# Optimization experiments

Hardware: AMD Instinct MI355X
Metric: run time of the kernel (lower is better)

The kernel has to match this reference:

```python
import jax, jax.numpy as jnp
import numpy as np

N_EXPERTS = 8
TOP_K = 2
D_MODEL = 1024
D_FF = 4 * D_MODEL

def setup_inputs() -> dict:
    key = jax.random.key(0)
    ks = jax.random.split(key, 5)
    s_in = 1.0 / np.sqrt(D_MODEL)
    s_ff = 1.0 / np.sqrt(D_FF)
    return {
        "x": jax.random.normal(ks[0], (2, 2048, D_MODEL), dtype=jnp.float32),
        "Wr": jax.random.normal(ks[1], (N_EXPERTS, D_MODEL), dtype=jnp.float32) * s_in,
        "W1": jax.random.normal(ks[2], (N_EXPERTS, D_FF, D_MODEL), dtype=jnp.float32) * s_in,
        "W2": jax.random.normal(ks[3], (N_EXPERTS, D_MODEL, D_FF), dtype=jnp.float32) * s_ff,
        "W3": jax.random.normal(ks[4], (N_EXPERTS, D_FF, D_MODEL), dtype=jnp.float32) * s_in,
    }

def reference(x, Wr, W1, W2, W3):
    B, S, D = x.shape
    T = B * S
    xf = x.reshape(T, D)
    logits = xf @ Wr.T                         # [T, E]
    probs = jax.nn.softmax(logits, axis=-1)
    top_p, top_i = jax.lax.top_k(probs, TOP_K)  # [T, K]
    top_p = top_p / jnp.sum(top_p, axis=-1, keepdims=True)
    # per-token combine weight for each expert: [T, E]
    onehot = jax.nn.one_hot(top_i, N_EXPERTS, dtype=x.dtype)  # [T, K, E]
    cw = jnp.einsum('tke,tk->te', onehot, top_p)
    out = jnp.zeros_like(xf)
    for e in range(N_EXPERTS):  # fixed small structural loop over experts
        h = jax.nn.silu(xf @ W1[e].T) * (xf @ W3[e].T)  # [T, F]
        y = h @ W2[e].T                                 # [T, D]
        out = out + cw[:, e:e+1] * y
    importance = jnp.sum(probs, axis=0)                 # [E]
    load = jnp.sum(jnp.sum(onehot, axis=1), axis=0)     # [E]
    aux_loss = jnp.sum(importance * load) * (N_EXPERTS / (T ** 2 + 1e-06))
    return out.reshape(B, S, D), aux_loss
```

## Files before the change

### kernel.cpp

```cpp
#include <hip/hip_runtime.h>

#define T_TOK 4096
#define DM 1024
#define DF 4096
#define NE 8
#define BM 128
#define BK 64
#define RCAP 9216
#define MAXT 72
#define CHUNK_B 8192
#define ACH_B 16384

typedef _Float16 f16x8 __attribute__((ext_vector_type(8)));
typedef float f32x4 __attribute__((ext_vector_type(4)));

#define MFMA16(a, b, c) __builtin_amdgcn_mfma_f32_16x16x32_f16(a, b, c, 0, 0, 0)

__device__ __forceinline__ ushort f2h_bits(float f) {
    _Float16 h = (_Float16)f;
    return __builtin_bit_cast(unsigned short, h);
}

__device__ __forceinline__ uint4 pack8(float4 a, float4 b) {
    union { ushort u[8]; uint4 v; } r;
    r.u[0] = f2h_bits(a.x); r.u[1] = f2h_bits(a.y);
    r.u[2] = f2h_bits(a.z); r.u[3] = f2h_bits(a.w);
    r.u[4] = f2h_bits(b.x); r.u[5] = f2h_bits(b.y);
    r.u[6] = f2h_bits(b.z); r.u[7] = f2h_bits(b.w);
    return r.v;
}

__device__ __forceinline__ void gll16(const void* g, void* l) {
    __builtin_amdgcn_global_load_lds(
        (const __attribute__((address_space(1))) unsigned int*)g,
        (__attribute__((address_space(3))) unsigned int*)l, 16, 0, 0);
}

__global__ __launch_bounds__(256) void k_init(float* __restrict__ out,
                                              int* __restrict__ misc,
                                              int* __restrict__ row_tok) {
    int i = blockIdx.x * 256 + threadIdx.x;
    if (i < T_TOK * DM + 1) out[i] = 0.f;
    if (i < RCAP) row_tok[i] = -1;
    if (i < 256) misc[i] = 0;
}

__global__ __launch_bounds__(64) void k_router(const float* __restrict__ x,
                                               const float* __restrict__ Wr,
                                               float* __restrict__ probs,
                                               int* __restrict__ topi,
                                               float* __restrict__ topw,
                                               int* __restrict__ cnt) {
    int t = blockIdx.x;
    int lane = threadIdx.x;
    const float* xr = x + (size_t)t * DM;
    float s[NE];
#pragma unroll
    for (int e = 0; e < NE; e++) s[e] = 0.f;
    for (int j = lane; j < DM; j += 64) {
        float xv = xr[j];
#pragma unroll
        for (int e = 0; e < NE; e++) s[e] += xv * Wr[e * DM + j];
    }
#pragma unroll
    for (int off = 32; off > 0; off >>= 1) {
#pragma unroll
        for (int e = 0; e < NE; e++) s[e] += __shfl_xor(s[e], off, 64);
    }
    if (lane == 0) {
        float mx = s[0];
#pragma unroll
        for (int e = 1; e < NE; e++) mx = fmaxf(mx, s[e]);
        float ex[NE], sum = 0.f;
#pragma unroll
        for (int e = 0; e < NE; e++) { ex[e] = expf(s[e] - mx); sum += ex[e]; }
        float inv = 1.f / sum;
        float p[NE];
#pragma unroll
        for (int e = 0; e < NE; e++) { p[e] = ex[e] * inv; probs[t * NE + e] = p[e]; }
        int i0 = 0;
#pragma unroll
        for (int e = 1; e < NE; e++) if (p[e] > p[i0]) i0 = e;
        int i1 = (i0 == 0) ? 1 : 0;
#pragma unroll
        for (int e = 0; e < NE; e++) if (e != i0 && p[e] > p[i1]) i1 = e;
        float w0 = p[i0], w1 = p[i1], winv = 1.f / (w0 + w1);
        topi[2 * t] = i0;     topw[2 * t] = w0 * winv;
        topi[2 * t + 1] = i1; topw[2 * t + 1] = w1 * winv;
        atomicAdd(&cnt[i0], 1);
        atomicAdd(&cnt[i1], 1);
    }
}

__global__ __launch_bounds__(256) void k_scan(const float* __restrict__ probs,
                                              const int* __restrict__ cnt,
                                              int* __restrict__ poff,
                                              int* __restrict__ texp,
                                              float* __restrict__ aux_out) {
    __shared__ float red[256 * NE];
    int tid = threadIdx.x;
    float part[NE];
#pragma unroll
    for (int e = 0; e < NE; e++) part[e] = 0.f;
    for (int t = tid; t < T_TOK; t += 256) {
#pragma unroll
        for (int e = 0; e < NE; e++) part[e] += probs[t * NE + e];
    }
#pragma unroll
    for (int e = 0; e < NE; e++) red[tid * NE + e] = part[e];
    __syncthreads();
    for (int s2 = 128; s2 > 0; s2 >>= 1) {
        if (tid < s2) {
#pragma unroll
            for (int e = 0; e < NE; e++) red[tid * NE + e] += red[(tid + s2) * NE + e];
        }
        __syncthreads();
    }
    if (tid == 0) {
        float al = 0.f;
#pragma unroll
        for (int e = 0; e < NE; e++) al += red[e] * (float)cnt[e];
        *aux_out = al * (8.0f / (16777216.0f + 1e-6f));
        int run = 0, tix = 0;
        for (int e = 0; e < NE; e++) {
            poff[e] = run;
            int nt = (cnt[e] + BM - 1) / BM;
            for (int i = 0; i < nt; i++) texp[tix++] = e;
            run += nt * BM;
        }
    }
}

__global__ __launch_bounds__(256) void k_assign(const int* __restrict__ topi,
                                                const float* __restrict__ topw,
                                                const int* __restrict__ poff,
                                                int* __restrict__ fill,
                                                int* __restrict__ row_tok,
                                                float* __restrict__ row_w) {
    int t = blockIdx.x * 256 + threadIdx.x;
    if (t >= T_TOK) return;
#pragma unroll
    for (int k = 0; k < 2; k++) {
        int e = topi[2 * t + k];
        int pos = atomicAdd(&fill[e], 1);
        int r = poff[e] + pos;
        row_tok[r] = t;
        row_w[r] = topw[2 * t + k];
    }
}

__global__ __launch_bounds__(256) void k_convert(const float* __restrict__ src,
                                                 ushort* __restrict__ dst,
                                                 int row_len) {
    int nk = row_len >> 6;
    int kt = blockIdx.x, rt = blockIdx.y;
    int tid = threadIdx.x;
    int r = tid >> 2, c0 = (tid & 3) * 16;
    const float* s = src + (size_t)(rt * 64 + r) * row_len + kt * 64 + c0;
    float4 v0 = *(const float4*)(s);
    float4 v1 = *(const float4*)(s + 4);
    float4 v2 = *(const float4*)(s + 8);
    float4 v3 = *(const float4*)(s + 12);
    char* chunk = (char*)dst + ((size_t)rt * nk + kt) * CHUNK_B;
    int sw = (r & 7) << 4;
    *(uint4*)(chunk + r * 128 + ((2 * c0) ^ sw)) = pack8(v0, v1);
    *(uint4*)(chunk + r * 128 + ((2 * c0 + 16) ^ sw)) = pack8(v2, v3);
}

__global__ __launch_bounds__(256) void k_gather_t(const float* __restrict__ x,
                                                  const int* __restrict__ row_tok,
                                                  ushort* __restrict__ xg) {
    int kt = blockIdx.x, rt = blockIdx.y;
    int tid = threadIdx.x;
    int r = tid >> 1, c0 = (tid & 1) * 32;
    int tok = row_tok[rt * BM + r];
    char* chunk = (char*)xg + ((size_t)rt * 16 + kt) * ACH_B;
    int sw = (r & 7) << 4;
    if (tok >= 0) {
        const float* s = x + (size_t)tok * DM + kt * 64 + c0;
#pragma unroll
        for (int j = 0; j < 4; j++) {
            float4 va = *(const float4*)(s + j * 8);
            float4 vb = *(const float4*)(s + j * 8 + 4);
            *(uint4*)(chunk + r * 128 + ((2 * (c0 + j * 8)) ^ sw)) = pack8(va, vb);
        }
    } else {
        uint4 z = {0, 0, 0, 0};
#pragma unroll
        for (int j = 0; j < 4; j++)
            *(uint4*)(chunk + r * 128 + ((2 * (c0 + j * 8)) ^ sw)) = z;
    }
}

__global__ __launch_bounds__(256) void k_gemm1_t(const ushort* __restrict__ xg,
                                                 const ushort* __restrict__ W1h,
                                                 const ushort* __restrict__ W3h,
                                                 const int* __restrict__ texp,
                                                 ushort* __restrict__ hbuf) {
    __shared__ __align__(16) char lA[2][16384];
    __shared__ __align__(16) char lB1[2][8192];
    __shared__ __align__(16) char lB3[2][8192];
    int ct = blockIdx.x, rt = blockIdx.y;
    int e = texp[rt];
    const char* Ac  = (const char*)xg + (size_t)rt * 16 * ACH_B;
    const char* B1c = (const char*)W1h + (size_t)((e * 64 + ct) * 16) * CHUNK_B;
    const char* B3c = (const char*)W3h + (size_t)((e * 64 + ct) * 16) * CHUNK_B;
    int tid = threadIdx.x, lane = tid & 63, wv = tid >> 6;
    int wr = wv >> 1, wc = wv & 1;

    const f32x4 fz = {0.f, 0.f, 0.f, 0.f};
    f32x4 acc1[4][2], acc3[4][2];
#pragma unroll
    for (int m = 0; m < 4; m++)
#pragma unroll
        for (int n = 0; n < 2; n++) { acc1[m][n] = fz; acc3[m][n] = fz; }

#define G1_STAGE(kt_, b_)                                                              \
    {                                                                                  \
        const char* As_  = Ac + (kt_) * ACH_B;                                         \
        const char* B1s_ = B1c + (kt_) * CHUNK_B;                                      \
        const char* B3s_ = B3c + (kt_) * CHUNK_B;                                      \
        _Pragma("unroll")                                                              \
        for (int i = 0; i < 4; i++)                                                    \
            gll16(As_ + wv * 4096 + i * 1024 + lane * 16, lA[b_] + wv * 4096 + i * 1024); \
        _Pragma("unroll")                                                              \
        for (int i = 0; i < 2; i++)                                                    \
            gll16(B1s_ + wv * 2048 + i * 1024 + lane * 16, lB1[b_] + wv * 2048 + i * 1024); \
        _Pragma("unroll")                                                              \
        for (int i = 0; i < 2; i++)                                                    \
            gll16(B3s_ + wv * 2048 + i * 1024 + lane * 16, lB3[b_] + wv * 2048 + i * 1024); \
    }

    G1_STAGE(0, 0);
    asm volatile("s_waitcnt vmcnt(0)" ::: "memory");
    __syncthreads();
    int cur = 0;
    for (int kt = 0; kt < 16; kt++) {
        if (kt < 15) G1_STAGE(kt + 1, cur ^ 1);
#pragma unroll
        for (int ks = 0; ks < 2; ks++) {
            int kbyte = (ks * 32 + (lane >> 4) * 8) * 2;
            f16x8 af[4];
#pragma unroll
            for (int m = 0; m < 4; m++) {
                int r = wr * 64 + m * 16 + (lane & 15);
                af[m] = *(const f16x8*)(lA[cur] + r * 128 + (kbyte ^ ((r & 7) << 4)));
            }
#pragma unroll
            for (int n = 0; n < 2; n++) {
                int c = wc * 32 + n * 16 + (lane & 15);
                int off = c * 128 + (kbyte ^ ((c & 7) << 4));
                f16x8 b1 = *(const f16x8*)(lB1[cur] + off);
                f16x8 b3 = *(const f16x8*)(lB3[cur] + off);
#pragma unroll
                for (int m = 0; m < 4; m++) {
                    acc1[m][n] = MFMA16(af[m], b1, acc1[m][n]);
                    acc3[m][n] = MFMA16(af[m], b3, acc3[m][n]);
                }
            }
        }
        asm volatile("s_waitcnt vmcnt(0)" ::: "memory");
        __syncthreads();
        cur ^= 1;
    }
#undef G1_STAGE
    char* hc = (char*)hbuf + (size_t)(rt * 64 + ct) * ACH_B;
#pragma unroll
    for (int m = 0; m < 4; m++) {
#pragma unroll
        for (int i = 0; i < 4; i++) {
            int r = wr * 64 + m * 16 + (lane >> 4) * 4 + i;
            int sw = (r & 7) << 4;
#pragma unroll
            for (int n = 0; n < 2; n++) {
                int f = wc * 32 + n * 16 + (lane & 15);
                float a1 = acc1[m][n][i], a3 = acc3[m][n][i];
                float h = (a1 / (1.f + expf(-a1))) * a3;
                *(ushort*)(hc + r * 128 + ((2 * f) ^ sw)) = f2h_bits(h);
            }
        }
    }
}

__global__ __launch_bounds__(256) void k_gemm2_t(const ushort* __restrict__ hbuf,
                                                 const ushort* __restrict__ W2h,
                                                 const int* __restrict__ texp,
                                                 const int* __restrict__ row_tok,
                                                 const float* __restrict__ row_w,
                                                 float* __restrict__ out) {
    __shared__ __align__(16) char lA[2][16384];
    __shared__ __align__(16) char lB[2][8192];
    int ct = blockIdx.x, rt = blockIdx.y;
    int e = texp[rt];
    const char* Ac = (const char*)hbuf + (size_t)rt * 64 * ACH_B;
    const char* Bc = (const char*)W2h + (size_t)((e * 16 + ct) * 64) * CHUNK_B;
    int tid = threadIdx.x, lane = tid & 63, wv = tid >> 6;
    int wr = wv >> 1, wc = wv & 1;

    const f32x4 fz = {0.f, 0.f, 0.f, 0.f};
    f32x4 acc[4][2];
#pragma unroll
    for (int m = 0; m < 4; m++)
#pragma unroll
        for (int n = 0; n < 2; n++) acc[m][n] = fz;

#define G2_STAGE(kt_, b_)                                                              \
    {                                                                                  \
        const char* As_ = Ac + (kt_) * ACH_B;                                          \
        const char* Bs_ = Bc + (kt_) * CHUNK_B;                                        \
        _Pragma("unroll")                                                              \
        for (int i = 0; i < 4; i++)                                                    \
            gll16(As_ + wv * 4096 + i * 1024 + lane * 16, lA[b_] + wv * 4096 + i * 1024); \
        _Pragma("unroll")                                                              \
        for (int i = 0; i < 2; i++)                                                    \
            gll16(Bs_ + wv * 2048 + i * 1024 + lane * 16, lB[b_] + wv * 2048 + i * 1024); \
    }

    G2_STAGE(0, 0);
    asm volatile("s_waitcnt vmcnt(0)" ::: "memory");
    __syncthreads();
    int cur = 0;
    for (int kt = 0; kt < 64; kt++) {
        if (kt < 63) G2_STAGE(kt + 1, cur ^ 1);
#pragma unroll
        for (int ks = 0; ks < 2; ks++) {
            int kbyte = (ks * 32 + (lane >> 4) * 8) * 2;
            f16x8 af[4];
#pragma unroll
            for (int m = 0; m < 4; m++) {
                int r = wr * 64 + m * 16 + (lane & 15);
                af[m] = *(const f16x8*)(lA[cur] + r * 128 + (kbyte ^ ((r & 7) << 4)));
            }
#pragma unroll
            for (int n = 0; n < 2; n++) {
                int c = wc * 32 + n * 16 + (lane & 15);
                f16x8 b = *(const f16x8*)(lB[cur] + c * 128 + (kbyte ^ ((c & 7) << 4)));
#pragma unroll
                for (int m = 0; m < 4; m++) acc[m][n] = MFMA16(af[m], b, acc[m][n]);
            }
        }
        asm volatile("s_waitcnt vmcnt(0)" ::: "memory");
        __syncthreads();
        cur ^= 1;
    }
#undef G2_STAGE
    int cbase = ct * 64 + wc * 32;
#pragma unroll
    for (int m = 0; m < 4; m++) {
#pragma unroll
        for (int i = 0; i < 4; i++) {
            int rr = rt * BM + wr * 64 + m * 16 + (lane >> 4) * 4 + i;
            int tok = row_tok[rr];
            if (tok >= 0) {
                float w = row_w[rr];
                float* orow = out + (size_t)tok * DM + cbase + (lane & 15);
#pragma unroll
                for (int n = 0; n < 2; n++) atomicAdd(&orow[n * 16], w * acc[m][n][i]);
            }
        }
    }
}

extern "C" void kernel_launch(void* const* d_in, const int* in_sizes, int n_in,
                              void* d_out, int out_size, void* d_ws, size_t ws_size,
                              hipStream_t stream) {
    (void)in_sizes; (void)n_in; (void)out_size; (void)ws_size;
    const float* x  = (const float*)d_in[0];
    const float* Wr = (const float*)d_in[1];
    const float* W1 = (const float*)d_in[2];
    const float* W2 = (const float*)d_in[3];
    const float* W3 = (const float*)d_in[4];
    float* out = (float*)d_out;
    char* ws = (char*)d_ws;

    int* misc = (int*)ws;
    int* cnt  = misc;
    int* fill = misc + 8;
    int* poff = misc + 16;
    int* texp = misc + 24;
    int*    topi    = (int*)(ws + 1024);
    float*  topw    = (float*)(ws + 33792);
    float*  probs   = (float*)(ws + 66560);
    int*    row_tok = (int*)(ws + 197632);
    float*  row_w   = (float*)(ws + 234496);
    ushort* xg      = (ushort*)(ws + 271360);
    ushort* hbuf    = (ushort*)(ws + 19145728);
    ushort* W1h     = (ushort*)(ws + 94643200);
    ushort* W3h     = (ushort*)(ws + 161752064);
    ushort* W2h     = (ushort*)(ws + 228860928);

    k_init<<<(T_TOK * DM + 1 + 255) / 256, 256, 0, stream>>>(out, misc, row_tok);
    k_router<<<T_TOK, 64, 0, stream>>>(x, Wr, probs, topi, topw, cnt);
    k_scan<<<1, 256, 0, stream>>>(probs, cnt, poff, texp, out + (size_t)T_TOK * DM);
    k_assign<<<(T_TOK + 255) / 256, 256, 0, stream>>>(topi, topw, poff, fill, row_tok, row_w);

    k_convert<<<dim3(16, 512), 256, 0, stream>>>(W1, W1h, DM);
    k_convert<<<dim3(16, 512), 256, 0, stream>>>(W3, W3h, DM);
    k_convert<<<dim3(64, 128), 256, 0, stream>>>(W2, W2h, DF);
    k_gather_t<<<dim3(16, MAXT), 256, 0, stream>>>(x, row_tok, xg);
    k_gemm1_t<<<dim3(64, MAXT), 256, 0, stream>>>(xg, W1h, W3h, texp, hbuf);
    k_gemm2_t<<<dim3(16, MAXT), 256, 0, stream>>>(hbuf, W2h, texp, row_tok, row_w, out);
}
```

Before: 746.5 us.

## Widen expert GEMM N-tiles, relax waitcnt pipelining, and raise MFMA priority

GEMM1 moves to 512-thread blocks that each cover 128 FF columns, so every loaded activation tile feeds twice as many columns. GEMM2 doubles the per-wave output width to 64 columns, with a 128-column block tile. Both kernels now wait on only the older load batch (partial vmcnt) before the barrier, so the next stage's prefetch overlaps compute. They also raise wave priority around the MFMA section. The cost is more LDS per block and more accumulator registers in GEMM2, which can reduce occupancy, and the grids shrink to half as many blocks.

```diff
diff --git a/kernel.cpp b/kernel.cpp
--- a/kernel.cpp
+++ b/kernel.cpp
@@ -5,7 +5,6 @@
 #define DF 4096
 #define NE 8
 #define BM 128
-#define BK 64
 #define RCAP 9216
 #define MAXT 72
 #define CHUNK_B 8192
@@ -192,21 +191,23 @@
     }
 }
 
-__global__ __launch_bounds__(256) void k_gemm1_t(const ushort* __restrict__ xg,
-                                                 const ushort* __restrict__ W1h,
-                                                 const ushort* __restrict__ W3h,
-                                                 const int* __restrict__ texp,
-                                                 ushort* __restrict__ hbuf) {
+__global__ __launch_bounds__(512, 2) void k_gemm1_t(const ushort* __restrict__ xg,
+                                                    const ushort* __restrict__ W1h,
+                                                    const ushort* __restrict__ W3h,
+                                                    const int* __restrict__ texp,
+                                                    ushort* __restrict__ hbuf) {
     __shared__ __align__(16) char lA[2][16384];
-    __shared__ __align__(16) char lB1[2][8192];
-    __shared__ __align__(16) char lB3[2][8192];
+    __shared__ __align__(16) char lB1[2][16384];
+    __shared__ __align__(16) char lB3[2][16384];
     int ct = blockIdx.x, rt = blockIdx.y;
     int e = texp[rt];
     const char* Ac  = (const char*)xg + (size_t)rt * 16 * ACH_B;
-    const char* B1c = (const char*)W1h + (size_t)((e * 64 + ct) * 16) * CHUNK_B;
-    const char* B3c = (const char*)W3h + (size_t)((e * 64 + ct) * 16) * CHUNK_B;
+    const char* B1c = (const char*)W1h + (size_t)((e * 64 + ct * 2) * 16) * CHUNK_B;
+    const char* B3c = (const char*)W3h + (size_t)((e * 64 + ct * 2) * 16) * CHUNK_B;
     int tid = threadIdx.x, lane = tid & 63, wv = tid >> 6;
-    int wr = wv >> 1, wc = wv & 1;
+    int wr = wv >> 2, wc = wv & 3;
+    int bch = wv >> 2;
+    int bin = (wv & 3) * 2048;
 
     const f32x4 fz = {0.f, 0.f, 0.f, 0.f};
     f32x4 acc1[4][2], acc3[4][2];
@@ -217,26 +218,31 @@
 
 #define G1_STAGE(kt_, b_)                                                              \
     {                                                                                  \
-        const char* As_  = Ac + (kt_) * ACH_B;                                         \
-        const char* B1s_ = B1c + (kt_) * CHUNK_B;                                      \
-        const char* B3s_ = B3c + (kt_) * CHUNK_B;                                      \
-        _Pragma("unroll")                                                              \
-        for (int i = 0; i < 4; i++)                                                    \
-            gll16(As_ + wv * 4096 + i * 1024 + lane * 16, lA[b_] + wv * 4096 + i * 1024); \
+        const char* As_ = Ac + (kt_) * ACH_B;                                          \
         _Pragma("unroll")                                                              \
         for (int i = 0; i < 2; i++)                                                    \
-            gll16(B1s_ + wv * 2048 + i * 1024 + lane * 16, lB1[b_] + wv * 2048 + i * 1024); \
+            gll16(As_ + wv * 2048 + i * 1024 + lane * 16, lA[b_] + wv * 2048 + i * 1024); \
+        const char* B1s_ = B1c + (size_t)(bch * 16 + (kt_)) * CHUNK_B + bin;           \
         _Pragma("unroll")                                                              \
         for (int i = 0; i < 2; i++)                                                    \
-            gll16(B3s_ + wv * 2048 + i * 1024 + lane * 16, lB3[b_] + wv * 2048 + i * 1024); \
+            gll16(B1s_ + i * 1024 + lane * 16, lB1[b_] + wv * 2048 + i * 1024);        \
+        const char* B3s_ = B3c + (size_t)(bch * 16 + (kt_)) * CHUNK_B + bin;           \
+        _Pragma("unroll")                                                              \
+        for (int i = 0; i < 2; i++)                                                    \
+            gll16(B3s_ + i * 1024 + lane * 16, lB3[b_] + wv * 2048 + i * 1024);        \
     }
 
     G1_STAGE(0, 0);
-    asm volatile("s_waitcnt vmcnt(0)" ::: "memory");
-    __syncthreads();
     int cur = 0;
     for (int kt = 0; kt < 16; kt++) {
-        if (kt < 15) G1_STAGE(kt + 1, cur ^ 1);
+        if (kt < 15) {
+            G1_STAGE(kt + 1, cur ^ 1);
+            asm volatile("s_waitcnt vmcnt(6)" ::: "memory");
+        } else {
+            asm volatile("s_waitcnt vmcnt(0)" ::: "memory");
+        }
+        __syncthreads();
+        __builtin_amdgcn_s_setprio(1);
 #pragma unroll
         for (int ks = 0; ks < 2; ks++) {
             int kbyte = (ks * 32 + (lane >> 4) * 8) * 2;
@@ -259,24 +265,24 @@
                 }
             }
         }
-        asm volatile("s_waitcnt vmcnt(0)" ::: "memory");
+        __builtin_amdgcn_s_setprio(0);
         __syncthreads();
         cur ^= 1;
     }
 #undef G1_STAGE
-    char* hc = (char*)hbuf + (size_t)(rt * 64 + ct) * ACH_B;
 #pragma unroll
     for (int m = 0; m < 4; m++) {
 #pragma unroll
         for (int i = 0; i < 4; i++) {
-            int r = wr * 64 + m * 16 + (lane >> 4) * 4 + i;
-            int sw = (r & 7) << 4;
+            int rl = wr * 64 + m * 16 + (lane >> 4) * 4 + i;
+            int sw = (rl & 7) << 4;
 #pragma unroll
             for (int n = 0; n < 2; n++) {
-                int f = wc * 32 + n * 16 + (lane & 15);
+                int fl = wc * 32 + n * 16 + (lane & 15);
                 float a1 = acc1[m][n][i], a3 = acc3[m][n][i];
                 float h = (a1 / (1.f + expf(-a1))) * a3;
-                *(ushort*)(hc + r * 128 + ((2 * f) ^ sw)) = f2h_bits(h);
+                char* hc = (char*)hbuf + ((size_t)rt * 64 + ct * 2 + (fl >> 6)) * ACH_B;
+                *(ushort*)(hc + rl * 128 + ((2 * (fl & 63)) ^ sw)) = f2h_bits(h);
             }
         }
     }
@@ -289,39 +295,46 @@
                                                  const float* __restrict__ row_w,
                                                  float* __restrict__ out) {
     __shared__ __align__(16) char lA[2][16384];
-    __shared__ __align__(16) char lB[2][8192];
+    __shared__ __align__(16) char lB[2][16384];
     int ct = blockIdx.x, rt = blockIdx.y;
     int e = texp[rt];
     const char* Ac = (const char*)hbuf + (size_t)rt * 64 * ACH_B;
-    const char* Bc = (const char*)W2h + (size_t)((e * 16 + ct) * 64) * CHUNK_B;
+    const char* Bc = (const char*)W2h + (size_t)((e * 16 + ct * 2) * 64) * CHUNK_B;
     int tid = threadIdx.x, lane = tid & 63, wv = tid >> 6;
     int wr = wv >> 1, wc = wv & 1;
+    int bch = wv >> 1;
+    int bin = (wv & 1) * 4096;
 
     const f32x4 fz = {0.f, 0.f, 0.f, 0.f};
-    f32x4 acc[4][2];
+    f32x4 acc[4][4];
 #pragma unroll
     for (int m = 0; m < 4; m++)
 #pragma unroll
-        for (int n = 0; n < 2; n++) acc[m][n] = fz;
+        for (int n = 0; n < 4; n++) acc[m][n] = fz;
 
 #define G2_STAGE(kt_, b_)                                                              \
     {                                                                                  \
         const char* As_ = Ac + (kt_) * ACH_B;                                          \
-        const char* Bs_ = Bc + (kt_) * CHUNK_B;                                        \
         _Pragma("unroll")                                                              \
         for (int i = 0; i < 4; i++)                                                    \
             gll16(As_ + wv * 4096 + i * 1024 + lane * 16, lA[b_] + wv * 4096 + i * 1024); \
+        const char* Bs_ = Bc + (size_t)(bch * 64 + (kt_)) * CHUNK_B + bin;             \
         _Pragma("unroll")                                                              \
-        for (int i = 0; i < 2; i++)                                                    \
-            gll16(Bs_ + wv * 2048 + i * 1024 + lane * 16, lB[b_] + wv * 2048 + i * 1024); \
+        for (int i = 0; i < 4; i++)                                                    \
+            gll16(Bs_ + i * 1024 + lane * 16, lB[b_] + wv * 4096 + i * 1024);          \
     }
 
     G2_STAGE(0, 0);
-    asm volatile("s_waitcnt vmcnt(0)" ::: "memory");
-    __syncthreads();
     int cur = 0;
     for (int kt = 0; kt < 64; kt++) {
-        if (kt < 63) G2_STAGE(kt + 1, cur ^ 1);
+        if (kt < 63) {
+            G2_STAGE(kt + 1, cur ^ 1);
+            asm volatile("s_waitcnt vmcnt(8)" ::: "memory");
+        } else {
+            asm volatile("s_waitcnt vmcnt(0)" ::: "memory");
+        }
+        __syncthreads();
+        __builtin_amdgcn_s_setprio(1);
 #pragma unroll
         for (int ks = 0; ks < 2; ks++) {
             int kbyte = (ks * 32 + (lane >> 4) * 8) * 2;
@@ -332,19 +345,19 @@
                 af[m] = *(const f16x8*)(lA[cur] + r * 128 + (kbyte ^ ((r & 7) << 4)));
             }
 #pragma unroll
-            for (int n = 0; n < 2; n++) {
-                int c = wc * 32 + n * 16 + (lane & 15);
+            for (int n = 0; n < 4; n++) {
+                int c = wc * 64 + n * 16 + (lane & 15);
                 f16x8 b = *(const f16x8*)(lB[cur] + c * 128 + (kbyte ^ ((c & 7) << 4)));
 #pragma unroll
                 for (int m = 0; m < 4; m++) acc[m][n] = MFMA16(af[m], b, acc[m][n]);
             }
         }
-        asm volatile("s_waitcnt vmcnt(0)" ::: "memory");
+        __builtin_amdgcn_s_setprio(0);
         __syncthreads();
         cur ^= 1;
     }
 #undef G2_STAGE
-    int cbase = ct * 64 + wc * 32;
+    int cbase = ct * 128 + wc * 64;
 #pragma unroll
     for (int m = 0; m < 4; m++) {
 #pragma unroll
@@ -355,7 +368,7 @@
                 float w = row_w[rr];
                 float* orow = out + (size_t)tok * DM + cbase + (lane & 15);
 #pragma unroll
-                for (int n = 0; n < 2; n++) atomicAdd(&orow[n * 16], w * acc[m][n][i]);
+                for (int n = 0; n < 4; n++) atomicAdd(&orow[n * 16], w * acc[m][n][i]);
             }
         }
     }
@@ -398,6 +411,6 @@
     k_convert<<<dim3(16, 512), 256, 0, stream>>>(W3, W3h, DM);
     k_convert<<<dim3(64, 128), 256, 0, stream>>>(W2, W2h, DF);
     k_gather_t<<<dim3(16, MAXT), 256, 0, stream>>>(x, row_tok, xg);
-    k_gemm1_t<<<dim3(64, MAXT), 256, 0, stream>>>(xg, W1h, W3h, texp, hbuf);
-    k_gemm2_t<<<dim3(16, MAXT), 256, 0, stream>>>(hbuf, W2h, texp, row_tok, row_w, out);
-}
+    k_gemm1_t<<<dim3(32, MAXT), 512, 0, stream>>>(xg, W1h, W3h, texp, hbuf);
+    k_gemm2_t<<<dim3(8, MAXT), 256, 0, stream>>>(hbuf, W2h, texp, row_tok, row_w, out);
+}
```

After: 771.3 us. +3.3%, slower.
